# Optimization experiments

Measured on AMD Instinct MI355X. Metric: run time of the kernel, lower is better.

Reference implementation:

```python
import jax, jax.numpy as jnp
import numpy as np

HIDDEN = 1024   # hidden_dimensions (dim_in)
NUM_HEADS = 16
HEAD_DIM = 64   # dim_q == dim_k == output_dimensions per head
BATCH = 4
SEQ = 2048


def setup_inputs() -> dict:
    key = jax.random.key(0)
    ks = jax.random.split(key, 11)
    s = 1.0 / np.sqrt(HIDDEN)
    so = 1.0 / np.sqrt(NUM_HEADS * HEAD_DIM)
    return {
        "Q": jax.random.normal(ks[0], (BATCH, SEQ, HIDDEN), jnp.float32),
        "K": jax.random.normal(ks[1], (BATCH, SEQ, HIDDEN), jnp.float32),
        "V": jax.random.normal(ks[2], (BATCH, SEQ, HIDDEN), jnp.float32),
        # per-head projection weights stacked over the head axis
        "Wq": jax.random.uniform(ks[3], (NUM_HEADS, HIDDEN, HEAD_DIM), jnp.float32, -s, s),
        "bq": jax.random.uniform(ks[4], (NUM_HEADS, HEAD_DIM), jnp.float32, -s, s),
        "Wk": jax.random.uniform(ks[5], (NUM_HEADS, HIDDEN, HEAD_DIM), jnp.float32, -s, s),
        "bk": jax.random.uniform(ks[6], (NUM_HEADS, HEAD_DIM), jnp.float32, -s, s),
        "Wv": jax.random.uniform(ks[7], (NUM_HEADS, HIDDEN, HEAD_DIM), jnp.float32, -s, s),
        "bv": jax.random.uniform(ks[8], (NUM_HEADS, HEAD_DIM), jnp.float32, -s, s),
        # output projection: concat(num_heads*head_dim) -> hidden
        "Wo": jax.random.uniform(ks[9], (NUM_HEADS * HEAD_DIM, HIDDEN), jnp.float32, -so, so),
        "bo": jax.random.uniform(ks[10], (HIDDEN,), jnp.float32, -so, so),
    }


def reference(Q, K, V, Wq, bq, Wk, bk, Wv, bv, Wo, bo):
    # Per-head linear projections (batched over heads instead of Python loop)
    q = jnp.einsum("bsd,hdk->bhsk", Q, Wq) + bq[None, :, None, :]  # [B,H,S,dk]
    k = jnp.einsum("bsd,hdk->bhsk", K, Wk) + bk[None, :, None, :]
    v = jnp.einsum("bsd,hdk->bhsk", V, Wv) + bv[None, :, None, :]
    # Scaled dot-product attention
    scale = 1.0 / jnp.sqrt(jnp.asarray(k.shape[-1], q.dtype))
    scores = jnp.einsum("bhqk,bhsk->bhqs", q, k) * scale          # [B,H,S,S]
    attn = jax.nn.softmax(scores, axis=-1)
    o = jnp.einsum("bhqs,bhsk->bhqk", attn, v)                     # [B,H,S,dk]
    # Concatenate heads along the feature dim, then output linear
    B, H, S, dk = o.shape
    concat = jnp.transpose(o, (0, 2, 1, 3)).reshape(B, S, H * dk)  # [B,S,H*dk]
    return concat @ Wo + bo                                        # [B,S,HIDDEN]
```

## Files before the change

kernel.cpp:

```cpp
#include <hip/hip_runtime.h>
#include <hip/hip_bf16.h>
#include <stdint.h>

typedef unsigned short u16;
typedef uint32_t u32;
typedef __attribute__((ext_vector_type(4))) float f32x4;
typedef __attribute__((ext_vector_type(16))) float f32x16;
typedef __attribute__((ext_vector_type(8))) short s8v;
typedef __attribute__((ext_vector_type(4))) unsigned short u16x4;
typedef __attribute__((ext_vector_type(2))) uint32_t u32x2;

#define SCALE_Q 0.18033688f

__device__ __forceinline__ u16 f2bf(float f) {
  union { float f; uint32_t u; } v; v.f = f;
  uint32_t r = v.u + 0x7fffu + ((v.u >> 16) & 1u);
  return (u16)(r >> 16);
}

__device__ __forceinline__ u32 pk2(float lo, float hi) {
  __hip_bfloat162 h = __float22bfloat162_rn(float2{lo, hi});
  union { __hip_bfloat162 h; u32 u; } c; c.h = h; return c.u;
}

__device__ __forceinline__ void gl16(const void* g, void* l) {
  __builtin_amdgcn_global_load_lds((const __attribute__((address_space(1))) u32*)g,
                                   (__attribute__((address_space(3))) u32*)l, 16, 0, 0);
}

__global__ __launch_bounds__(256) void k_conv3(const float* __restrict__ a, const float* __restrict__ b,
                                               const float* __restrict__ c, u16* __restrict__ oa,
                                               u16* __restrict__ ob, u16* __restrict__ oc) {
  int which = blockIdx.y;
  const float* in = which == 0 ? a : (which == 1 ? b : c);
  u16* out = which == 0 ? oa : (which == 1 ? ob : oc);
  int i = (blockIdx.x * 256 + threadIdx.x) * 4;
  float4 v = *(const float4*)(in + i);
  u16x4 o; o[0] = f2bf(v.x); o[1] = f2bf(v.y); o[2] = f2bf(v.z); o[3] = f2bf(v.w);
  *(u16x4*)(out + i) = o;
}

__global__ __launch_bounds__(256) void k_convW_t(const float* __restrict__ wq, const float* __restrict__ wk,
                                                 const float* __restrict__ wv, u16* __restrict__ oq,
                                                 u16* __restrict__ ok, u16* __restrict__ ov) {
  __shared__ float T[64][65];
  const int z = blockIdx.z, h = blockIdx.y, d0 = blockIdx.x * 64;
  const float* w = z == 0 ? wq : (z == 1 ? wk : wv);
  u16* o = z == 0 ? oq : (z == 1 ? ok : ov);
  const float scale = z == 0 ? SCALE_Q : 1.0f;
  const int t = threadIdx.x;
#pragma unroll
  for (int i = 0; i < 16; ++i) {
    int f = t + i * 256;
    T[f >> 6][f & 63] = w[(h * 1024 + d0 + (f >> 6)) * 64 + (f & 63)];
  }
  __syncthreads();
#pragma unroll
  for (int i = 0; i < 16; ++i) {
    int g = t + i * 256;
    o[(h * 64 + (g >> 6)) * 1024 + d0 + (g & 63)] = f2bf(T[g & 63][g >> 6] * scale);
  }
}

__global__ __launch_bounds__(256) void k_convWo_t(const float* __restrict__ w, u16* __restrict__ o) {
  __shared__ float T[64][65];
  const int n0 = blockIdx.x * 64, c0 = blockIdx.y * 64;
  const int t = threadIdx.x;
#pragma unroll
  for (int i = 0; i < 16; ++i) {
    int f = t + i * 256;
    T[f >> 6][f & 63] = w[(c0 + (f >> 6)) * 1024 + n0 + (f & 63)];
  }
  __syncthreads();
#pragma unroll
  for (int i = 0; i < 16; ++i) {
    int g = t + i * 256;
    o[(n0 + (g >> 6)) * 1024 + c0 + (g & 63)] = f2bf(T[g & 63][g >> 6]);
  }
}

__global__ __launch_bounds__(256) void k_gemm3(
    const u16* __restrict__ Aq, const u16* __restrict__ Ak, const u16* __restrict__ Av,
    const u16* __restrict__ Bq, const u16* __restrict__ Bk, const u16* __restrict__ Bv,
    const float* __restrict__ bqp, const float* __restrict__ bkp, const float* __restrict__ bvp,
    u16* __restrict__ oq, u16* __restrict__ ok, u16* __restrict__ ov) {
  constexpr int Kd = 1024, Nd = 1024;
  __shared__ alignas(16) u16 As[2][128 * 64];
  __shared__ alignas(16) u16 Bs[2][128 * 64];
  const int z = blockIdx.z;
  const u16* A = z == 0 ? Aq : (z == 1 ? Ak : Av);
  const u16* Bt = z == 0 ? Bq : (z == 1 ? Bk : Bv);
  const float* bias = z == 0 ? bqp : (z == 1 ? bkp : bvp);

  const int t = threadIdx.x;
  const int lane = t & 63;
  const int w = t >> 6;
  const int wm = w >> 1, wn = w & 1;
  const int lr = lane & 15, lg = lane >> 4;
  const long bm = blockIdx.x * 128, bn = blockIdx.y * 128;
  const int r8 = lane >> 3, c8 = lane & 7;
  const int chunk = c8 ^ r8;

  f32x4 acc[4][4] = {};
  const u16* Ap = A + (bm + w * 8 + r8) * (long)Kd + chunk * 8;
  const u16* Bp = Bt + (bn + w * 8 + r8) * (long)Kd + chunk * 8;

  auto GSTAGE = [&](u16* Asb, u16* Bsb, int kt) {
#pragma unroll
    for (int p = 0; p < 4; ++p) {
      gl16(Ap + (long)p * 32 * Kd + kt, Asb + (p * 32 + w * 8) * 64);
      gl16(Bp + (long)p * 32 * Kd + kt, Bsb + (p * 32 + w * 8) * 64);
    }
  };
  auto GCOMP = [&](const u16* Asb, const u16* Bsb) {
#pragma unroll
    for (int ks = 0; ks < 2; ++ks) {
      s8v af[4], bf[4];
#pragma unroll
      for (int i = 0; i < 4; ++i) {
        int arow = wm * 64 + i * 16 + lr;
        af[i] = *(const s8v*)(Asb + arow * 64 + (((ks * 4 + lg) ^ (arow & 7)) * 8));
        int brow = wn * 64 + i * 16 + lr;
        bf[i] = *(const s8v*)(Bsb + brow * 64 + (((ks * 4 + lg) ^ (brow & 7)) * 8));
      }
#pragma unroll
      for (int i = 0; i < 4; ++i)
#pragma unroll
        for (int j = 0; j < 4; ++j)
          acc[i][j] = __builtin_amdgcn_mfma_f32_16x16x32_bf16(af[i], bf[j], acc[i][j], 0, 0, 0);
    }
  };

  GSTAGE(As[0], Bs[0], 0);
  __syncthreads();
  for (int kt = 0; kt < Kd; kt += 128) {
    if (kt + 64 < Kd) GSTAGE(As[1], Bs[1], kt + 64);
    GCOMP(As[0], Bs[0]);
    __syncthreads();
    if (kt + 128 < Kd) GSTAGE(As[0], Bs[0], kt + 128);
    GCOMP(As[1], Bs[1]);
    __syncthreads();
  }

  const float bscale = z == 0 ? SCALE_Q : 1.0f;
  float bcol[4];
#pragma unroll
  for (int j = 0; j < 4; ++j) bcol[j] = bias[bn + wn * 64 + j * 16 + lr] * bscale;

  if (z < 2) {
    u16* C = z == 0 ? oq : ok;
#pragma unroll
    for (int i = 0; i < 4; ++i) {
      long m0 = bm + wm * 64 + i * 16 + lg * 4;
#pragma unroll
      for (int j = 0; j < 4; ++j) {
        long n = bn + wn * 64 + j * 16 + lr;
#pragma unroll
        for (int r = 0; r < 4; ++r)
          C[(m0 + r) * Nd + n] = f2bf(acc[i][j][r] + bcol[j]);
      }
    }
  } else {
    u16* C = ov;
    int lgp = ((lg & 1) << 1) | (lg >> 1);
#pragma unroll
    for (int i = 0; i < 4; ++i) {
      long m0 = bm + wm * 64 + i * 16 + lgp * 4;
      int b = (int)(m0 >> 11), s0 = (int)(m0 & 2047);
#pragma unroll
      for (int j = 0; j < 4; ++j) {
        int n = (int)(bn + wn * 64 + j * 16 + lr);
        int h = n >> 6, dv = n & 63;
        u32x2 cc;
        cc[0] = pk2(acc[i][j][0] + bcol[j], acc[i][j][1] + bcol[j]);
        cc[1] = pk2(acc[i][j][2] + bcol[j], acc[i][j][3] + bcol[j]);
        *(u32x2*)(C + (long)((b * 16 + h) * 64 + dv) * 2048 + s0) = cc;
      }
    }
  }
}

__global__ __launch_bounds__(256) void k_gemmo(const u16* __restrict__ A, const u16* __restrict__ Bt,
                                               const float* __restrict__ bias, float* __restrict__ C) {
  constexpr int Kd = 1024, Nd = 1024;
  __shared__ alignas(16) u16 As[2][128 * 64];
  __shared__ alignas(16) u16 Bs[2][128 * 64];
  const int t = threadIdx.x;
  const int lane = t & 63;
  const int w = t >> 6;
  const int wm = w >> 1, wn = w & 1;
  const int lr = lane & 15, lg = lane >> 4;
  const long bm = blockIdx.x * 128, bn = blockIdx.y * 128;
  const int r8 = lane >> 3, c8 = lane & 7;
  const int chunk = c8 ^ r8;

  f32x4 acc[4][4] = {};
  const u16* Ap = A + (bm + w * 8 + r8) * (long)Kd + chunk * 8;
  const u16* Bp = Bt + (bn + w * 8 + r8) * (long)Kd + chunk * 8;

  auto GSTAGE = [&](u16* Asb, u16* Bsb, int kt) {
#pragma unroll
    for (int p = 0; p < 4; ++p) {
      gl16(Ap + (long)p * 32 * Kd + kt, Asb + (p * 32 + w * 8) * 64);
      gl16(Bp + (long)p * 32 * Kd + kt, Bsb + (p * 32 + w * 8) * 64);
    }
  };
  auto GCOMP = [&](const u16* Asb, const u16* Bsb) {
#pragma unroll
    for (int ks = 0; ks < 2; ++ks) {
      s8v af[4], bf[4];
#pragma unroll
      for (int i = 0; i < 4; ++i) {
        int arow = wm * 64 + i * 16 + lr;
        af[i] = *(const s8v*)(Asb + arow * 64 + (((ks * 4 + lg) ^ (arow & 7)) * 8));
        int brow = wn * 64 + i * 16 + lr;
        bf[i] = *(const s8v*)(Bsb + brow * 64 + (((ks * 4 + lg) ^ (brow & 7)) * 8));
      }
#pragma unroll
      for (int i = 0; i < 4; ++i)
#pragma unroll
        for (int j = 0; j < 4; ++j)
          acc[i][j] = __builtin_amdgcn_mfma_f32_16x16x32_bf16(af[i], bf[j], acc[i][j], 0, 0, 0);
    }
  };

  GSTAGE(As[0], Bs[0], 0);
  __syncthreads();
  for (int kt = 0; kt < Kd; kt += 128) {
    if (kt + 64 < Kd) GSTAGE(As[1], Bs[1], kt + 64);
    GCOMP(As[0], Bs[0]);
    __syncthreads();
    if (kt + 128 < Kd) GSTAGE(As[0], Bs[0], kt + 128);
    GCOMP(As[1], Bs[1]);
    __syncthreads();
  }

  float bcol[4];
#pragma unroll
  for (int j = 0; j < 4; ++j) bcol[j] = bias[bn + wn * 64 + j * 16 + lr];
#pragma unroll
  for (int i = 0; i < 4; ++i) {
    long m0 = bm + wm * 64 + i * 16 + lg * 4;
#pragma unroll
    for (int j = 0; j < 4; ++j) {
      long n = bn + wn * 64 + j * 16 + lr;
#pragma unroll
      for (int r = 0; r < 4; ++r)
        C[(m0 + r) * Nd + n] = acc[i][j][r] + bcol[j];
    }
  }
}

__global__ __launch_bounds__(512, 4) void k_attn(const u16* __restrict__ q, const u16* __restrict__ k,
                                                 const u16* __restrict__ vT, u16* __restrict__ o) {
  __shared__ alignas(16) u16 Ks[2][64 * 64];
  __shared__ alignas(16) u16 Vs[2][64 * 64];
  const int t = threadIdx.x;
  const int lane = t & 63;
  const int wv = t >> 6;
  const int l5 = lane & 31, hi = lane >> 5;
  const int qt = blockIdx.x, h = blockIdx.y, b = blockIdx.z;
  const int r8 = lane >> 3, c8 = lane & 7;
  const int rx = l5 & 7;

  const int qrow = qt * 256 + wv * 32 + l5;
  const u16* qp = q + ((long)(b * 2048 + qrow) * 1024 + h * 64);
  s8v qf[4];
#pragma unroll
  for (int s = 0; s < 4; ++s) qf[s] = *(const s8v*)(qp + s * 16 + hi * 8);

  const u16* Kpp = k + (long)b * 2048 * 1024 + h * 64 + (long)(wv * 8 + r8) * 1024 + ((c8 ^ r8) * 8);
  const u16* Vpp = vT + (long)(b * 16 + h) * 131072 + (long)(wv * 8 + r8) * 2048 + ((c8 ^ r8) * 8);

  f32x16 acc0 = {}, acc1 = {};
  float l_loc = 0.f;

  auto ASTAGE = [&](u16* ksd, u16* vsd, int kv) {
    gl16(Kpp + (long)kv * 1024, ksd + (wv * 8) * 64);
    gl16(Vpp + kv,              vsd + (wv * 8) * 64);
  };

  auto ATILE = [&](const u16* Ksb, const u16* Vsb) {
    f32x16 sa0 = {}, sa1 = {};
#pragma unroll
    for (int s = 0; s < 4; ++s) {
      int cw = 2 * s + hi;
      s8v kf0 = *(const s8v*)(Ksb + l5 * 64 + ((cw ^ rx) * 8));
      s8v kf1 = *(const s8v*)(Ksb + (32 + l5) * 64 + ((cw ^ rx) * 8));
      sa0 = __builtin_amdgcn_mfma_f32_32x32x16_bf16(kf0, qf[s], sa0, 0, 0, 0);
      sa1 = __builtin_amdgcn_mfma_f32_32x32x16_bf16(kf1, qf[s], sa1, 0, 0, 0);
    }
    u32 Ppk[16];
#pragma unroll
    for (int kb = 0; kb < 2; ++kb) {
#pragma unroll
      for (int r1 = 0; r1 < 4; ++r1) {
        float p0 = __builtin_amdgcn_exp2f(kb ? sa1[4 * r1 + 0] : sa0[4 * r1 + 0]);
        float p1 = __builtin_amdgcn_exp2f(kb ? sa1[4 * r1 + 1] : sa0[4 * r1 + 1]);
        float p2 = __builtin_amdgcn_exp2f(kb ? sa1[4 * r1 + 2] : sa0[4 * r1 + 2]);
        float p3 = __builtin_amdgcn_exp2f(kb ? sa1[4 * r1 + 3] : sa0[4 * r1 + 3]);
        l_loc += (p0 + p1) + (p2 + p3);
        Ppk[kb * 8 + r1 * 2 + 0] = pk2(p0, p1);
        Ppk[kb * 8 + r1 * 2 + 1] = pk2(p2, p3);
      }
    }
#pragma unroll
    for (int s2 = 0; s2 < 4; ++s2) {
      union { s8v v; u32 w[4]; } pu;
      pu.w[0] = Ppk[4 * s2 + 0]; pu.w[1] = Ppk[4 * s2 + 1];
      pu.w[2] = Ppk[4 * s2 + 2]; pu.w[3] = Ppk[4 * s2 + 3];
      int cw = 2 * s2 + hi;
      s8v vf0 = *(const s8v*)(Vsb + l5 * 64 + ((cw ^ rx) * 8));
      s8v vf1 = *(const s8v*)(Vsb + (32 + l5) * 64 + ((cw ^ rx) * 8));
      acc0 = __builtin_amdgcn_mfma_f32_32x32x16_bf16(vf0, pu.v, acc0, 0, 0, 0);
      acc1 = __builtin_amdgcn_mfma_f32_32x32x16_bf16(vf1, pu.v, acc1, 0, 0, 0);
    }
  };

  ASTAGE(Ks[0], Vs[0], 0);
  for (int kv = 0; kv < 2048; kv += 128) {
    __syncthreads();
    if (kv + 64 < 2048) ASTAGE(Ks[1], Vs[1], kv + 64);
    ATILE(Ks[0], Vs[0]);
    __syncthreads();
    if (kv + 128 < 2048) ASTAGE(Ks[0], Vs[0], kv + 128);
    ATILE(Ks[1], Vs[1]);
  }

  l_loc += __shfl_xor(l_loc, 32);
  float inv = 1.0f / l_loc;
  u16* op = o + ((long)(b * 2048 + qrow) * 1024 + h * 64);
#pragma unroll
  for (int kb = 0; kb < 2; ++kb) {
#pragma unroll
    for (int r1 = 0; r1 < 4; ++r1) {
      u32x2 cc;
      float a0 = kb ? acc1[4 * r1 + 0] : acc0[4 * r1 + 0];
      float a1 = kb ? acc1[4 * r1 + 1] : acc0[4 * r1 + 1];
      float a2 = kb ? acc1[4 * r1 + 2] : acc0[4 * r1 + 2];
      float a3 = kb ? acc1[4 * r1 + 3] : acc0[4 * r1 + 3];
      cc[0] = pk2(a0 * inv, a1 * inv);
      cc[1] = pk2(a2 * inv, a3 * inv);
      *(u32x2*)(op + kb * 32 + r1 * 8 + hi * 4) = cc;
    }
  }
}

extern "C" void kernel_launch(void* const* d_in, const int* in_sizes, int n_in,
                              void* d_out, int out_size, void* d_ws, size_t ws_size,
                              hipStream_t stream) {
  const float* Q  = (const float*)d_in[0];
  const float* K  = (const float*)d_in[1];
  const float* V  = (const float*)d_in[2];
  const float* Wq = (const float*)d_in[3];
  const float* bq = (const float*)d_in[4];
  const float* Wk = (const float*)d_in[5];
  const float* bk = (const float*)d_in[6];
  const float* Wv = (const float*)d_in[7];
  const float* bvp = (const float*)d_in[8];
  const float* Wo = (const float*)d_in[9];
  const float* bo = (const float*)d_in[10];
  float* out = (float*)d_out;

  char* ws = (char*)d_ws;
  const size_t MB16 = (size_t)8192 * 1024 * 2;
  u16* Qb  = (u16*)(ws);
  u16* Kb  = (u16*)(ws + MB16);
  u16* Vb  = (u16*)(ws + 2 * MB16);
  u16* WqT = (u16*)(ws + 3 * MB16);
  u16* WkT = (u16*)(ws + 3 * MB16 + ((size_t)2 << 20));
  u16* WvT = (u16*)(ws + 3 * MB16 + ((size_t)4 << 20));
  u16* WoT = (u16*)(ws + 3 * MB16 + ((size_t)6 << 20));
  u16* qws = (u16*)(ws + 3 * MB16 + ((size_t)8 << 20));
  u16* kws = (u16*)(ws + 4 * MB16 + ((size_t)8 << 20));
  u16* vTs = (u16*)(ws + 5 * MB16 + ((size_t)8 << 20));
  u16* ows = Qb;

  k_conv3<<<dim3(8192, 3), 256, 0, stream>>>(Q, K, V, Qb, Kb, Vb);
  k_convW_t<<<dim3(16, 16, 3), 256, 0, stream>>>(Wq, Wk, Wv, WqT, WkT, WvT);
  k_convWo_t<<<dim3(16, 16), 256, 0, stream>>>(Wo, WoT);

  k_gemm3<<<dim3(64, 8, 3), 256, 0, stream>>>(Qb, Kb, Vb, WqT, WkT, WvT,
                                              bq, bk, bvp, qws, kws, vTs);

  k_attn<<<dim3(8, 16, 4), 512, 0, stream>>>(qws, kws, vTs, ows);

  k_gemmo<<<dim3(64, 8), 256, 0, stream>>>(ows, WoT, bo, out);
}
```

Before: 219.2 us.

## Restructure attention into 4-stage pipeline with two Q tiles per wave

```diff
diff --git a/kernel.cpp b/kernel.cpp
--- a/kernel.cpp
+++ b/kernel.cpp
@@ -27,6 +27,9 @@
   __builtin_amdgcn_global_load_lds((const __attribute__((address_space(1))) u32*)g,
                                    (__attribute__((address_space(3))) u32*)l, 16, 0, 0);
 }
+
+#define BARRIER()  __builtin_amdgcn_s_barrier()
+#define SCHEDB()   __builtin_amdgcn_sched_barrier(0)
 
 __global__ __launch_bounds__(256) void k_conv3(const float* __restrict__ a, const float* __restrict__ b,
                                                const float* __restrict__ c, u16* __restrict__ oa,
@@ -132,14 +135,19 @@
   };
 
   GSTAGE(As[0], Bs[0], 0);
-  __syncthreads();
-  for (int kt = 0; kt < Kd; kt += 128) {
-    if (kt + 64 < Kd) GSTAGE(As[1], Bs[1], kt + 64);
-    GCOMP(As[0], Bs[0]);
-    __syncthreads();
-    if (kt + 128 < Kd) GSTAGE(As[0], Bs[0], kt + 128);
-    GCOMP(As[1], Bs[1]);
-    __syncthreads();
+  for (int kt = 0; kt < 16; ++kt) {
+    BARRIER();
+    SCHEDB();
+    if (kt < 15) {
+      GSTAGE(As[(kt + 1) & 1], Bs[(kt + 1) & 1], (kt + 1) * 64);
+      asm volatile("s_waitcnt vmcnt(8)" ::: "memory");
+    } else {
+      asm volatile("s_waitcnt vmcnt(0)" ::: "memory");
+    }
+    SCHEDB();
+    BARRIER();
+    SCHEDB();
+    GCOMP(As[kt & 1], Bs[kt & 1]);
   }
 
   const float bscale = z == 0 ? SCALE_Q : 1.0f;
@@ -225,14 +233,19 @@
   };
 
   GSTAGE(As[0], Bs[0], 0);
-  __syncthreads();
-  for (int kt = 0; kt < Kd; kt += 128) {
-    if (kt + 64 < Kd) GSTAGE(As[1], Bs[1], kt + 64);
-    GCOMP(As[0], Bs[0]);
-    __syncthreads();
-    if (kt + 128 < Kd) GSTAGE(As[0], Bs[0], kt + 128);
-    GCOMP(As[1], Bs[1]);
-    __syncthreads();
+  for (int kt = 0; kt < 16; ++kt) {
+    BARRIER();
+    SCHEDB();
+    if (kt < 15) {
+      GSTAGE(As[(kt + 1) & 1], Bs[(kt + 1) & 1], (kt + 1) * 64);
+      asm volatile("s_waitcnt vmcnt(8)" ::: "memory");
+    } else {
+      asm volatile("s_waitcnt vmcnt(0)" ::: "memory");
+    }
+    SCHEDB();
+    BARRIER();
+    SCHEDB();
+    GCOMP(As[kt & 1], Bs[kt & 1]);
   }
 
   float bcol[4];
@@ -251,97 +264,154 @@
   }
 }
 
-__global__ __launch_bounds__(512, 4) void k_attn(const u16* __restrict__ q, const u16* __restrict__ k,
+__global__ __launch_bounds__(256, 2) void k_attn(const u16* __restrict__ q, const u16* __restrict__ k,
                                                  const u16* __restrict__ vT, u16* __restrict__ o) {
-  __shared__ alignas(16) u16 Ks[2][64 * 64];
-  __shared__ alignas(16) u16 Vs[2][64 * 64];
+  __shared__ alignas(16) u16 Ks[4][64 * 64];
+  __shared__ alignas(16) u16 Vs[4][64 * 64];
   const int t = threadIdx.x;
   const int lane = t & 63;
   const int wv = t >> 6;
   const int l5 = lane & 31, hi = lane >> 5;
-  const int qt = blockIdx.x, h = blockIdx.y, b = blockIdx.z;
   const int r8 = lane >> 3, c8 = lane & 7;
   const int rx = l5 & 7;
 
-  const int qrow = qt * 256 + wv * 32 + l5;
-  const u16* qp = q + ((long)(b * 2048 + qrow) * 1024 + h * 64);
-  s8v qf[4];
-#pragma unroll
-  for (int s = 0; s < 4; ++s) qf[s] = *(const s8v*)(qp + s * 16 + hi * 8);
-
-  const u16* Kpp = k + (long)b * 2048 * 1024 + h * 64 + (long)(wv * 8 + r8) * 1024 + ((c8 ^ r8) * 8);
-  const u16* Vpp = vT + (long)(b * 16 + h) * 131072 + (long)(wv * 8 + r8) * 2048 + ((c8 ^ r8) * 8);
-
-  f32x16 acc0 = {}, acc1 = {};
-  float l_loc = 0.f;
-
-  auto ASTAGE = [&](u16* ksd, u16* vsd, int kv) {
-    gl16(Kpp + (long)kv * 1024, ksd + (wv * 8) * 64);
-    gl16(Vpp + kv,              vsd + (wv * 8) * 64);
-  };
-
-  auto ATILE = [&](const u16* Ksb, const u16* Vsb) {
-    f32x16 sa0 = {}, sa1 = {};
+  const int wg = blockIdx.x;
+  const int ob = (wg & 7) * 64 + (wg >> 3);
+  const int qt = ob & 7, h = (ob >> 3) & 15, b = ob >> 7;
+
+  const int qrow0 = qt * 256 + wv * 64 + l5;
+  const u16* qpA = q + ((long)(b * 2048 + qrow0) * 1024 + h * 64);
+  const u16* qpB = qpA + 32 * 1024;
+  s8v qfA[4], qfB[4];
+#pragma unroll
+  for (int s = 0; s < 4; ++s) {
+    qfA[s] = *(const s8v*)(qpA + s * 16 + hi * 8);
+    qfB[s] = *(const s8v*)(qpB + s * 16 + hi * 8);
+  }
+
+  const u16* Kpp = k + (long)b * 2048 * 1024 + h * 64 + (long)r8 * 1024 + ((c8 ^ r8) * 8);
+  const u16* Vpp = vT + (long)(b * 16 + h) * 131072 + (long)r8 * 2048 + ((c8 ^ r8) * 8);
+
+  f32x16 accA0 = {}, accA1 = {}, accB0 = {}, accB1 = {};
+  float lA = 0.f, lB = 0.f;
+
+  int offs[4];
+#pragma unroll
+  for (int s = 0; s < 4; ++s) offs[s] = ((2 * s + hi) ^ rx) * 8;
+  const int rb0 = l5 * 64, rb1 = rb0 + 2048;
+
+  auto ASTAGE = [&](int buf, int kv) {
+#pragma unroll
+    for (int r0 = 0; r0 < 2; ++r0) {
+      int rowo = wv * 16 + r0 * 8;
+      gl16(Kpp + ((long)kv + rowo) * 1024, &Ks[buf][rowo * 64]);
+      gl16(Vpp + (long)rowo * 2048 + kv,   &Vs[buf][rowo * 64]);
+    }
+  };
+
+  auto ATILE = [&](int buf) {
+    const u16* Ksb = Ks[buf];
+    const u16* Vsb = Vs[buf];
+    s8v kf0[4], kf1[4];
 #pragma unroll
     for (int s = 0; s < 4; ++s) {
-      int cw = 2 * s + hi;
-      s8v kf0 = *(const s8v*)(Ksb + l5 * 64 + ((cw ^ rx) * 8));
-      s8v kf1 = *(const s8v*)(Ksb + (32 + l5) * 64 + ((cw ^ rx) * 8));
-      sa0 = __builtin_amdgcn_mfma_f32_32x32x16_bf16(kf0, qf[s], sa0, 0, 0, 0);
-      sa1 = __builtin_amdgcn_mfma_f32_32x32x16_bf16(kf1, qf[s], sa1, 0, 0, 0);
-    }
-    u32 Ppk[16];
+      kf0[s] = *(const s8v*)(Ksb + rb0 + offs[s]);
+      kf1[s] = *(const s8v*)(Ksb + rb1 + offs[s]);
+    }
+    f32x16 sA0 = {}, sA1 = {}, sB0 = {}, sB1 = {};
+    __builtin_amdgcn_s_setprio(1);
+#pragma unroll
+    for (int s = 0; s < 4; ++s) {
+      sA0 = __builtin_amdgcn_mfma_f32_32x32x16_bf16(kf0[s], qfA[s], sA0, 0, 0, 0);
+      sA1 = __builtin_amdgcn_mfma_f32_32x32x16_bf16(kf1[s], qfA[s], sA1, 0, 0, 0);
+      sB0 = __builtin_amdgcn_mfma_f32_32x32x16_bf16(kf0[s], qfB[s], sB0, 0, 0, 0);
+      sB1 = __builtin_amdgcn_mfma_f32_32x32x16_bf16(kf1[s], qfB[s], sB1, 0, 0, 0);
+    }
+    __builtin_amdgcn_s_setprio(0);
+    u32 PA[16], PB[16];
 #pragma unroll
     for (int kb = 0; kb < 2; ++kb) {
 #pragma unroll
       for (int r1 = 0; r1 < 4; ++r1) {
-        float p0 = __builtin_amdgcn_exp2f(kb ? sa1[4 * r1 + 0] : sa0[4 * r1 + 0]);
-        float p1 = __builtin_amdgcn_exp2f(kb ? sa1[4 * r1 + 1] : sa0[4 * r1 + 1]);
-        float p2 = __builtin_amdgcn_exp2f(kb ? sa1[4 * r1 + 2] : sa0[4 * r1 + 2]);
-        float p3 = __builtin_amdgcn_exp2f(kb ? sa1[4 * r1 + 3] : sa0[4 * r1 + 3]);
-        l_loc += (p0 + p1) + (p2 + p3);
-        Ppk[kb * 8 + r1 * 2 + 0] = pk2(p0, p1);
-        Ppk[kb * 8 + r1 * 2 + 1] = pk2(p2, p3);
+        float a0 = __builtin_amdgcn_exp2f(kb ? sA1[4 * r1 + 0] : sA0[4 * r1 + 0]);
+        float a1 = __builtin_amdgcn_exp2f(kb ? sA1[4 * r1 + 1] : sA0[4 * r1 + 1]);
+        float a2 = __builtin_amdgcn_exp2f(kb ? sA1[4 * r1 + 2] : sA0[4 * r1 + 2]);
+        float a3 = __builtin_amdgcn_exp2f(kb ? sA1[4 * r1 + 3] : sA0[4 * r1 + 3]);
+        lA += (a0 + a1) + (a2 + a3);
+        PA[kb * 8 + r1 * 2 + 0] = pk2(a0, a1);
+        PA[kb * 8 + r1 * 2 + 1] = pk2(a2, a3);
+        float b0 = __builtin_amdgcn_exp2f(kb ? sB1[4 * r1 + 0] : sB0[4 * r1 + 0]);
+        float b1 = __builtin_amdgcn_exp2f(kb ? sB1[4 * r1 + 1] : sB0[4 * r1 + 1]);
+        float b2 = __builtin_amdgcn_exp2f(kb ? sB1[4 * r1 + 2] : sB0[4 * r1 + 2]);
+        float b3 = __builtin_amdgcn_exp2f(kb ? sB1[4 * r1 + 3] : sB0[4 * r1 + 3]);
+        lB += (b0 + b1) + (b2 + b3);
+        PB[kb * 8 + r1 * 2 + 0] = pk2(b0, b1);
+        PB[kb * 8 + r1 * 2 + 1] = pk2(b2, b3);
       }
     }
+    __builtin_amdgcn_s_setprio(1);
 #pragma unroll
     for (int s2 = 0; s2 < 4; ++s2) {
-      union { s8v v; u32 w[4]; } pu;
-      pu.w[0] = Ppk[4 * s2 + 0]; pu.w[1] = Ppk[4 * s2 + 1];
-      pu.w[2] = Ppk[4 * s2 + 2]; pu.w[3] = Ppk[4 * s2 + 3];
-      int cw = 2 * s2 + hi;
-      s8v vf0 = *(const s8v*)(Vsb + l5 * 64 + ((cw ^ rx) * 8));
-      s8v vf1 = *(const s8v*)(Vsb + (32 + l5) * 64 + ((cw ^ rx) * 8));
-      acc0 = __builtin_amdgcn_mfma_f32_32x32x16_bf16(vf0, pu.v, acc0, 0, 0, 0);
-      acc1 = __builtin_amdgcn_mfma_f32_32x32x16_bf16(vf1, pu.v, acc1, 0, 0, 0);
-    }
-  };
-
-  ASTAGE(Ks[0], Vs[0], 0);
-  for (int kv = 0; kv < 2048; kv += 128) {
-    __syncthreads();
-    if (kv + 64 < 2048) ASTAGE(Ks[1], Vs[1], kv + 64);
-    ATILE(Ks[0], Vs[0]);
-    __syncthreads();
-    if (kv + 128 < 2048) ASTAGE(Ks[0], Vs[0], kv + 128);
-    ATILE(Ks[1], Vs[1]);
-  }
-
-  l_loc += __shfl_xor(l_loc, 32);
-  float inv = 1.0f / l_loc;
-  u16* op = o + ((long)(b * 2048 + qrow) * 1024 + h * 64);
+      union { s8v v; u32 w[4]; } pa, pb;
+      pa.w[0] = PA[4 * s2 + 0]; pa.w[1] = PA[4 * s2 + 1];
+      pa.w[2] = PA[4 * s2 + 2]; pa.w[3] = PA[4 * s2 + 3];
+      pb.w[0] = PB[4 * s2 + 0]; pb.w[1] = PB[4 * s2 + 1];
+      pb.w[2] = PB[4 * s2 + 2]; pb.w[3] = PB[4 * s2 + 3];
+      s8v vf0 = *(const s8v*)(Vsb + rb0 + offs[s2]);
+      s8v vf1 = *(const s8v*)(Vsb + rb1 + offs[s2]);
+      accA0 = __builtin_amdgcn_mfma_f32_32x32x16_bf16(vf0, pa.v, accA0, 0, 0, 0);
+      accA1 = __builtin_amdgcn_mfma_f32_32x32x16_bf16(vf1, pa.v, accA1, 0, 0, 0);
+      accB0 = __builtin_amdgcn_mfma_f32_32x32x16_bf16(vf0, pb.v, accB0, 0, 0, 0);
+      accB1 = __builtin_amdgcn_mfma_f32_32x32x16_bf16(vf1, pb.v, accB1, 0, 0, 0);
+    }
+    __builtin_amdgcn_s_setprio(0);
+  };
+
+  ASTAGE(0, 0);
+  ASTAGE(1, 64);
+  asm volatile("s_waitcnt vmcnt(4)" ::: "memory");
+  SCHEDB();
+  BARRIER();
+  SCHEDB();
+  for (int tt = 0; tt < 30; ++tt) {
+    ASTAGE((tt + 2) & 3, (tt + 2) * 64);
+    ATILE(tt & 3);
+    asm volatile("s_waitcnt vmcnt(4) lgkmcnt(0)" ::: "memory");
+    SCHEDB();
+    BARRIER();
+    SCHEDB();
+  }
+  ATILE(30 & 3);
+  asm volatile("s_waitcnt vmcnt(0) lgkmcnt(0)" ::: "memory");
+  SCHEDB();
+  BARRIER();
+  SCHEDB();
+  ATILE(31 & 3);
+
+  lA += __shfl_xor(lA, 32);
+  lB += __shfl_xor(lB, 32);
+  float iA = 1.0f / lA, iB = 1.0f / lB;
+  u16* opA = o + ((long)(b * 2048 + qrow0) * 1024 + h * 64);
+  u16* opB = opA + 32 * 1024;
 #pragma unroll
   for (int kb = 0; kb < 2; ++kb) {
 #pragma unroll
     for (int r1 = 0; r1 < 4; ++r1) {
-      u32x2 cc;
-      float a0 = kb ? acc1[4 * r1 + 0] : acc0[4 * r1 + 0];
-      float a1 = kb ? acc1[4 * r1 + 1] : acc0[4 * r1 + 1];
-      float a2 = kb ? acc1[4 * r1 + 2] : acc0[4 * r1 + 2];
-      float a3 = kb ? acc1[4 * r1 + 3] : acc0[4 * r1 + 3];
-      cc[0] = pk2(a0 * inv, a1 * inv);
-      cc[1] = pk2(a2 * inv, a3 * inv);
-      *(u32x2*)(op + kb * 32 + r1 * 8 + hi * 4) = cc;
+      u32x2 ca, cb;
+      float a0 = kb ? accA1[4 * r1 + 0] : accA0[4 * r1 + 0];
+      float a1 = kb ? accA1[4 * r1 + 1] : accA0[4 * r1 + 1];
+      float a2 = kb ? accA1[4 * r1 + 2] : accA0[4 * r1 + 2];
+      float a3 = kb ? accA1[4 * r1 + 3] : accA0[4 * r1 + 3];
+      ca[0] = pk2(a0 * iA, a1 * iA);
+      ca[1] = pk2(a2 * iA, a3 * iA);
+      *(u32x2*)(opA + kb * 32 + r1 * 8 + hi * 4) = ca;
+      float b0 = kb ? accB1[4 * r1 + 0] : accB0[4 * r1 + 0];
+      float b1 = kb ? accB1[4 * r1 + 1] : accB0[4 * r1 + 1];
+      float b2 = kb ? accB1[4 * r1 + 2] : accB0[4 * r1 + 2];
+      float b3 = kb ? accB1[4 * r1 + 3] : accB0[4 * r1 + 3];
+      cb[0] = pk2(b0 * iB, b1 * iB);
+      cb[1] = pk2(b2 * iB, b3 * iB);
+      *(u32x2*)(opB + kb * 32 + r1 * 8 + hi * 4) = cb;
     }
   }
 }
@@ -383,7 +453,7 @@
   k_gemm3<<<dim3(64, 8, 3), 256, 0, stream>>>(Qb, Kb, Vb, WqT, WkT, WvT,
                                               bq, bk, bvp, qws, kws, vTs);
 
-  k_attn<<<dim3(8, 16, 4), 512, 0, stream>>>(qws, kws, vTs, ows);
+  k_attn<<<dim3(512), 256, 0, stream>>>(qws, kws, vTs, ows);
 
   k_gemmo<<<dim3(64, 8), 256, 0, stream>>>(ows, WoT, bo, out);
 }
```

Result: faster. 204.7 us (-6.6%).
